# Kernel optimization log

Measured on AMD Instinct MI355X. Metric: run time of the kernel, lower is better.

Reference implementation:

```python
import jax, jax.numpy as jnp
import numpy as np

KH, KW = 3, 3  # window_size[1], window_size[2]
FILTERS = 64
CHANNELS = 32
K = KH * KW * CHANNELS


def _extract_patches_valid(x, kh, kw):
    # TF tf.image.extract_patches ordering: (row_offset, col_offset, channel)
    B, H, W, C = x.shape
    Ho, Wo = H - kh + 1, W - kw + 1
    cols = [x[:, i:i + Ho, j:j + Wo, :] for i in range(kh) for j in range(kw)]
    return jnp.concatenate(cols, axis=-1)  # (B, Ho, Wo, kh*kw*C)


def setup_inputs() -> dict:
    key = jax.random.key(0)
    kx, kw = jax.random.split(key)
    x = jax.random.normal(kx, (8, 32, 32, CHANNELS), dtype=jnp.float32)
    # learned weight per __init__: shape (1, 1, 1, K, filters), random_normal init
    w = jax.random.normal(kw, (1, 1, 1, K, FILTERS), dtype=jnp.float32) * 0.05
    return {"x": x, "w": w}


def reference(x, w):
    # patches: (B, Ho, Wo, K)
    patches = _extract_patches_valid(x, KH, KW)
    # broadcast-add against weights: (B, Ho, Wo, K, filters)
    s = patches[..., None] + w[0, 0, 0]  # w[0,0,0]: (K, filters)
    # tropical conv: max over patch axis minus min over patch axis
    return jnp.max(s, axis=3) - jnp.min(s, axis=3)  # (B, Ho, Wo, filters)
```

## Files before the change

kernel.cpp:

```cpp
#include <hip/hip_runtime.h>


#define C_IN 32
#define NF 64
#define H_OUT 30
#define W_OUT 30
#define W_IN 32

static __device__ __forceinline__ float max3f(float a, float b, float c) {
    return fmaxf(fmaxf(a, b), c);
}
static __device__ __forceinline__ float min3f(float a, float b, float c) {
    return fminf(fminf(a, b), c);
}

__global__ __launch_bounds__(512) void tropconv_kernel(
    const float* __restrict__ x,
    const float* __restrict__ w,
    float* __restrict__ out) {
    const int bx = blockIdx.x;
    const int q = bx & 3;
    const int bho = bx >> 2;
    const int b = bho / H_OUT;
    const int ho = bho - b * H_OUT;
    const int tid = threadIdx.x;
    const int lane = tid & 63;
    const int wave = tid >> 6;

    const int col0 = q * 8;
    const int npx = (q == 3) ? 6 : 8;
    const int ncols = (q == 3) ? 8 : 10;

    __shared__ __align__(16) float xs[3 * 10 * C_IN];
    __shared__ __align__(16) float pms[8][8][NF][2];

    {
        const int nf4_row = ncols * (C_IN / 4);
        const int total_f4 = 3 * nf4_row;
        if (tid < total_f4) {
            const int r = tid / nf4_row;
            const int cc = tid - r * nf4_row;
            const float4* __restrict__ src = (const float4*)(
                x + ((size_t)((b * 32 + ho + r) * W_IN + col0)) * C_IN);
            ((float4*)xs)[r * 80 + cc] = src[cc];
        }
    }

    __syncthreads();

    float mx[8], mn[8];
    #pragma unroll
    for (int t = 0; t < 8; ++t) { mx[t] = -INFINITY; mn[t] = INFINITY; }

    const float* __restrict__ wrow = w + (size_t)(wave * 4) * NF + lane;
    const float* xrow = xs + wave * 4;

    #pragma unroll 1
    for (int r = 0; r < 3; ++r) {
        float wr[12];
        #pragma unroll
        for (int t = 0; t < 12; ++t)
            wr[t] = wrow[((t >> 2) * C_IN + (t & 3)) * NF];

        #pragma unroll
        for (int cc = 0; cc < 10; ++cc) {
            const float4 p = *(const float4*)(xrow + cc * C_IN);
            #pragma unroll
            for (int j = 0; j < 3; ++j) {
                const int px = cc - j;
                if (px >= 0 && px < 8) {
                    float s0 = p.x + wr[j * 4 + 0];
                    float s1 = p.y + wr[j * 4 + 1];
                    float s2 = p.z + wr[j * 4 + 2];
                    float s3 = p.w + wr[j * 4 + 3];
                    mx[px] = max3f(max3f(s0, s1, s2), s3, mx[px]);
                    mn[px] = min3f(min3f(s0, s1, s2), s3, mn[px]);
                }
            }
        }
        wrow += 3 * C_IN * NF;
        xrow += 10 * C_IN;
    }

    #pragma unroll
    for (int px = 0; px < 8; ++px) {
        float2 v; v.x = mx[px]; v.y = mn[px];
        *(float2*)&pms[wave][px][lane][0] = v;
    }
    __syncthreads();

    if (tid < npx * 32) {
        const int px = tid >> 5;
        const int fp = tid & 31;
        float4 v0 = *(const float4*)&pms[0][px][fp * 2][0];
        float a0 = v0.x, m0 = v0.y, a1 = v0.z, m1 = v0.w;
        #pragma unroll
        for (int ww = 1; ww < 8; ++ww) {
            const float4 v = *(const float4*)&pms[ww][px][fp * 2][0];
            a0 = fmaxf(a0, v.x); m0 = fminf(m0, v.y);
            a1 = fmaxf(a1, v.z); m1 = fminf(m1, v.w);
        }
        float2 o; o.x = a0 - m0; o.y = a1 - m1;
        *(float2*)&out[((size_t)bho * W_OUT + (col0 + px)) * NF + fp * 2] = o;
    }
}

extern "C" void kernel_launch(void* const* d_in, const int* in_sizes, int n_in,
                              void* d_out, int out_size, void* d_ws, size_t ws_size,
                              hipStream_t stream) {
    const float* x = (const float*)d_in[0];
    const float* w = (const float*)d_in[1];
    float* out = (float*)d_out;

    dim3 grid(8 * H_OUT * 4);
    dim3 block(512);
    tropconv_kernel<<<grid, block, 0, stream>>>(x, w, out);
}
```

Measured before the change: 63.80 us.

## Load input directly from global memory and prefetch next weight rows

Removes the LDS staging of the input tile and the barrier that follows it. Each wave now reads its float4 input slices straight from global memory (broadcast across lanes, clamped at the right edge), and the weights for the next kernel row are loaded while the current row is computed. This cuts a synchronization and LDS traffic but adds register pressure and redundant global loads across waves that rely on cache hits.

New measurement: 66.13 us. 3.6% more time.

```diff
diff --git a/kernel.cpp b/kernel.cpp
--- a/kernel.cpp
+++ b/kernel.cpp
@@ -29,42 +29,44 @@
 
     const int col0 = q * 8;
     const int npx = (q == 3) ? 6 : 8;
-    const int ncols = (q == 3) ? 8 : 10;
 
-    __shared__ __align__(16) float xs[3 * 10 * C_IN];
     __shared__ __align__(16) float pms[8][8][NF][2];
 
-    {
-        const int nf4_row = ncols * (C_IN / 4);
-        const int total_f4 = 3 * nf4_row;
-        if (tid < total_f4) {
-            const int r = tid / nf4_row;
-            const int cc = tid - r * nf4_row;
-            const float4* __restrict__ src = (const float4*)(
-                x + ((size_t)((b * 32 + ho + r) * W_IN + col0)) * C_IN);
-            ((float4*)xs)[r * 80 + cc] = src[cc];
-        }
-    }
-
-    __syncthreads();
+    const float* __restrict__ xb =
+        x + (size_t)((b * 32 + ho) * W_IN) * C_IN + wave * 4;
 
     float mx[8], mn[8];
     #pragma unroll
     for (int t = 0; t < 8; ++t) { mx[t] = -INFINITY; mn[t] = INFINITY; }
 
-    const float* __restrict__ wrow = w + (size_t)(wave * 4) * NF + lane;
-    const float* xrow = xs + wave * 4;
+    const float* __restrict__ wlane = w + (size_t)(wave * 4) * NF + lane;
+
+    float wr[12];
+    #pragma unroll
+    for (int t = 0; t < 12; ++t)
+        wr[t] = wlane[((t >> 2) * C_IN + (t & 3)) * NF];
 
     #pragma unroll 1
     for (int r = 0; r < 3; ++r) {
-        float wr[12];
+        float4 xv[10];
+        const float* __restrict__ xr = xb + (size_t)r * W_IN * C_IN;
         #pragma unroll
-        for (int t = 0; t < 12; ++t)
-            wr[t] = wrow[((t >> 2) * C_IN + (t & 3)) * NF];
+        for (int c = 0; c < 10; ++c) {
+            int col = col0 + c;
+            col = (col < 31) ? col : 31;
+            xv[c] = *(const float4*)(xr + col * C_IN);
+        }
+
+        float wn[12];
+        if (r < 2) {
+            #pragma unroll
+            for (int t = 0; t < 12; ++t)
+                wn[t] = wlane[(((r + 1) * 3 + (t >> 2)) * C_IN + (t & 3)) * NF];
+        }
 
         #pragma unroll
         for (int cc = 0; cc < 10; ++cc) {
-            const float4 p = *(const float4*)(xrow + cc * C_IN);
+            const float4 p = xv[cc];
             #pragma unroll
             for (int j = 0; j < 3; ++j) {
                 const int px = cc - j;
@@ -78,8 +80,11 @@
                 }
             }
         }
-        wrow += 3 * C_IN * NF;
-        xrow += 10 * C_IN;
+
+        if (r < 2) {
+            #pragma unroll
+            for (int t = 0; t < 12; ++t) wr[t] = wn[t];
+        }
     }
 
     #pragma unroll
```
